# Optimization experiments

Measured on AMD Instinct MI355X. Metric: run time of the kernel, lower is better.

## Reference

```python
import jax, jax.numpy as jnp
import numpy as np


def setup_inputs() -> dict:
    key = jax.random.key(0)
    k1, k2 = jax.random.split(key)
    data = jax.random.normal(k1, (1000000, 64), dtype=jnp.float32)
    # unique, in-range indices (ONNX ScatterND is undefined for duplicates)
    indices = jnp.arange(100000, dtype=jnp.int64 if jax.config.jax_enable_x64 else jnp.int32).reshape(100000, 1)
    updates = jax.random.normal(k2, (100000, 64), dtype=jnp.float32)
    return {"data": data, "indices": indices, "updates": updates}


def reference(data, indices, updates):
    # ONNX ScatterND with k = indices.shape[-1] = 1: scatter rows of `updates`
    # into a copy of `data` at row positions indices[..., 0].
    rows = indices[..., 0]  # [num_updates]
    return data.at[rows].set(updates)
```

## Files before the change

### kernel.cpp

```cpp
#include <hip/hip_runtime.h>
#include <stdint.h>


typedef float f32x4 __attribute__((ext_vector_type(4)));

__global__ __launch_bounds__(256) void copy_flat_kernel(
    const f32x4* __restrict__ src, f32x4* __restrict__ dst, size_t n4) {
    const size_t i = (size_t)blockIdx.x * blockDim.x + threadIdx.x;
    if (i < n4) dst[i] = src[i];
}

__global__ __launch_bounds__(256) void scatter_flat_kernel(
    const int* __restrict__ idx,
    const f32x4* __restrict__ upd,
    f32x4* __restrict__ out,
    size_t total4) {
    const size_t i = (size_t)blockIdx.x * blockDim.x + threadIdx.x;
    if (i < total4) {
        const size_t row = i >> 4;
        const size_t col = i & 15;
        const int r = idx[row];
        out[(size_t)r * 16 + col] = upd[i];
    }
}

extern "C" void kernel_launch(void* const* d_in, const int* in_sizes, int n_in,
                              void* d_out, int out_size, void* d_ws, size_t ws_size,
                              hipStream_t stream) {
    const float* data    = (const float*)d_in[0];
    const int*   indices = (const int*)d_in[1];
    const float* updates = (const float*)d_in[2];
    float* out = (float*)d_out;

    const size_t n4          = (size_t)out_size / 4;
    const size_t num_updates = (size_t)in_sizes[2] / 64;
    const size_t total4      = num_updates * 16;

    const int block = 256;
    const int gc = (int)((n4 + block - 1) / block);
    const int gs = (int)((total4 + block - 1) / block);

    copy_flat_kernel<<<gc, block, 0, stream>>>(
        (const f32x4*)data, (f32x4*)out, n4);
    scatter_flat_kernel<<<gs, block, 0, stream>>>(
        indices, (const f32x4*)updates, (f32x4*)out, total4);
}
```

Measured before the change: 99.88 us.

## Mark scattered rows in a flag buffer and skip copying them

Scatters updates first while writing a per-row byte flag into workspace, then copies data only into rows that were not overwritten. This avoids writing output rows twice: once from data and once from updates. It adds a flag-zeroing kernel, a third launch and a flag read per vector in the copy. The old path remains as a fallback when the workspace is too small or the row count is not a multiple of 16.

```diff
diff --git a/kernel.cpp b/kernel.cpp
--- a/kernel.cpp
+++ b/kernel.cpp
@@ -3,6 +3,38 @@
 
 
 typedef float f32x4 __attribute__((ext_vector_type(4)));
+typedef uint32_t u32x4 __attribute__((ext_vector_type(4)));
+
+__global__ __launch_bounds__(256) void zero_flags_kernel(
+    u32x4* __restrict__ p, size_t n16) {
+    const size_t i = (size_t)blockIdx.x * blockDim.x + threadIdx.x;
+    if (i < n16) p[i] = (u32x4){0u, 0u, 0u, 0u};
+}
+
+__global__ __launch_bounds__(256) void scatter_flag_kernel(
+    const int* __restrict__ idx,
+    const f32x4* __restrict__ upd,
+    f32x4* __restrict__ out,
+    uint8_t* __restrict__ flags,
+    size_t total4) {
+    const size_t i = (size_t)blockIdx.x * blockDim.x + threadIdx.x;
+    if (i < total4) {
+        const size_t row = i >> 4;
+        const size_t col = i & 15;
+        const int r = idx[row];
+        out[(size_t)r * 16 + col] = upd[i];
+        if (col == 0) flags[r] = 1;
+    }
+}
+
+__global__ __launch_bounds__(256) void copy_skip_kernel(
+    const f32x4* __restrict__ src,
+    f32x4* __restrict__ dst,
+    const uint8_t* __restrict__ flags,
+    size_t n4) {
+    const size_t i = (size_t)blockIdx.x * blockDim.x + threadIdx.x;
+    if (i < n4 && !flags[i >> 4]) dst[i] = src[i];
+}
 
 __global__ __launch_bounds__(256) void copy_flat_kernel(
     const f32x4* __restrict__ src, f32x4* __restrict__ dst, size_t n4) {
@@ -33,15 +65,28 @@
     float* out = (float*)d_out;
 
     const size_t n4          = (size_t)out_size / 4;
+    const size_t num_rows    = (size_t)out_size / 64;
     const size_t num_updates = (size_t)in_sizes[2] / 64;
     const size_t total4      = num_updates * 16;
 
     const int block = 256;
-    const int gc = (int)((n4 + block - 1) / block);
-    const int gs = (int)((total4 + block - 1) / block);
+    auto blocks_for = [&](size_t work) {
+        return (int)((work + block - 1) / block);
+    };
 
-    copy_flat_kernel<<<gc, block, 0, stream>>>(
-        (const f32x4*)data, (f32x4*)out, n4);
-    scatter_flat_kernel<<<gs, block, 0, stream>>>(
-        indices, (const f32x4*)updates, (f32x4*)out, total4);
+    if (ws_size >= num_rows && (num_rows % 16) == 0) {
+        uint8_t* flags = (uint8_t*)d_ws;
+        const size_t n16 = num_rows / 16;
+        zero_flags_kernel<<<blocks_for(n16), block, 0, stream>>>(
+            (u32x4*)flags, n16);
+        scatter_flag_kernel<<<blocks_for(total4), block, 0, stream>>>(
+            indices, (const f32x4*)updates, (f32x4*)out, flags, total4);
+        copy_skip_kernel<<<blocks_for(n4), block, 0, stream>>>(
+            (const f32x4*)data, (f32x4*)out, flags, n4);
+    } else {
+        copy_flat_kernel<<<blocks_for(n4), block, 0, stream>>>(
+            (const f32x4*)data, (f32x4*)out, n4);
+        scatter_flat_kernel<<<blocks_for(total4), block, 0, stream>>>(
+            indices, (const f32x4*)updates, (f32x4*)out, total4);
+    }
 }
```

Measured after the change: 99.20 us. About the same (-0.7%).
